# Kernel optimization log

Measured on AMD Instinct MI355X. Metric: run time of the kernel, lower is better.

The kernel has to match this reference:

```python
import jax, jax.numpy as jnp
import numpy as np
from jax import lax

B, T, P, H, L = 64, 1024, 256, 1024, 4  # batch, seq, proj(=input), cell, layers
SCALE = 1.0 / np.sqrt(H)


def _lstm_layer(x, Wih, Whh, bih, bhh, Whr):
    """One LSTM layer with projection. x: [B,T,in]. Returns h sequence [B,T,P]."""
    # Precompute input contribution to all 4 gates for all timesteps: [B,T,4H]
    xg = jnp.einsum('bti,gi->btg', x, Wih) + bih + bhh

    def step(carry, xg_t):
        h, c = carry                       # h:[B,P], c:[B,H]
        g = xg_t + h @ Whh.T               # [B,4H]
        i, f, gg, o = jnp.split(g, 4, axis=-1)  # torch gate order: i,f,g,o
        c = jax.nn.sigmoid(f) * c + jax.nn.sigmoid(i) * jnp.tanh(gg)
        h = (jax.nn.sigmoid(o) * jnp.tanh(c)) @ Whr.T  # projection -> [B,P]
        return (h, c), h

    h0 = jnp.zeros((x.shape[0], Whr.shape[0]), dtype=x.dtype)
    c0 = jnp.zeros((x.shape[0], Whr.shape[1]), dtype=x.dtype)
    _, ys = lax.scan(step, (h0, c0), jnp.swapaxes(xg, 0, 1))  # scan over time
    return jnp.swapaxes(ys, 0, 1)  # [B,T,P]


def setup_inputs() -> dict:
    key = jax.random.key(0)
    ks = jax.random.split(key, 7)
    return {
        'y': jax.random.normal(ks[0], (B, T, P), dtype=jnp.float32),
        'W_ih': jax.random.normal(ks[1], (L, 4 * H, P), dtype=jnp.float32) * SCALE,
        'W_hh': jax.random.normal(ks[2], (L, 4 * H, P), dtype=jnp.float32) * SCALE,
        'b_ih': jax.random.normal(ks[3], (L, 4 * H), dtype=jnp.float32) * SCALE,
        'b_hh': jax.random.normal(ks[4], (L, 4 * H), dtype=jnp.float32) * SCALE,
        'W_hr': jax.random.normal(ks[5], (L, P, H), dtype=jnp.float32) * SCALE,
        'min_seq_len': 1,
    }


def reference(y, W_ih, W_hh, b_ih, b_hh, W_hr, min_seq_len):
    x = y
    for l in range(L):  # small fixed layer count; dropout=0.1 is eval-mode identity
        x = _lstm_layer(x, W_ih[l], W_hh[l], b_ih[l], b_hh[l], W_hr[l])
    return x[:, min_seq_len:]
```

## Files before the change

### kernel.cpp

```cpp
#include <hip/hip_runtime.h>


#define B_    64
#define T_    1024
#define P_    256
#define H_    1024
#define L_    4
#define G4_   4096
#define NTHR  256
#define WWIN  8
#define HSLOT (P_ * B_)

#define LDS_FLOATS 37892
#define LDS_BYTES  (LDS_FLOATS * 4)

#define PA_CH  36
#define PA_BUF (64 * PA_CH)
#define PW_OFF (2 * PA_BUF)
#define PW_BUF (4 * PA_CH)

#define ACT_FLOATS ((size_t)L_ * H_ * B_)
#define WDOG_CAP 200000

struct alignas(16) F4 { float f[4]; };
typedef __attribute__((ext_vector_type(8))) short s8v;
typedef __attribute__((ext_vector_type(4))) float f4v;

__device__ __forceinline__ void lda2(const float* p, float& a, float& b) {
  union { double d; float f[2]; } u;
  u.d = __hip_atomic_load((const double*)p, __ATOMIC_RELAXED,
                          __HIP_MEMORY_SCOPE_AGENT);
  a = u.f[0]; b = u.f[1];
}
__device__ __forceinline__ void sta2(float* p, float a, float b) {
  union { double d; float f[2]; } u;
  u.f[0] = a; u.f[1] = b;
  __hip_atomic_store((double*)p, u.d, __ATOMIC_RELAXED,
                     __HIP_MEMORY_SCOPE_AGENT);
}
__device__ __forceinline__ void sta(float* p, float v) {
  __hip_atomic_store(p, v, __ATOMIC_RELAXED, __HIP_MEMORY_SCOPE_AGENT);
}
__device__ __forceinline__ void drain_vm() {
  asm volatile("s_waitcnt vmcnt(0)" ::: "memory");
}
__device__ __forceinline__ void bar_lds() {
  asm volatile("s_waitcnt lgkmcnt(0)\n\ts_barrier" ::: "memory");
}

__device__ __forceinline__ float fsig(float x) {
  float e = __expf(-x);
  return __builtin_amdgcn_rcpf(1.0f + e);
}
__device__ __forceinline__ float ftanh(float x) {
  float ax = fabsf(x);
  float e  = __expf(-2.0f * ax);
  float r  = (1.0f - e) * __builtin_amdgcn_rcpf(1.0f + e);
  return copysignf(r, x);
}
__device__ __forceinline__ ushort bf16_rne(float f) {
  uint u = __float_as_uint(f);
  uint r = u + 0x7FFFu + ((u >> 16) & 1u);
  return (ushort)(r >> 16);
}
__device__ __forceinline__ float bf16_to_f(ushort h) {
  return __uint_as_float(((uint)h) << 16);
}
__device__ __forceinline__ int wait1(int* f, int tid, int target, int* abrt,
                                     int self) {
  if (tid < 64) {
    int it = 0;
    while (true) {
      int v = (tid == self) ? 0x7fffffff
            : __hip_atomic_load(&f[tid], __ATOMIC_RELAXED, __HIP_MEMORY_SCOPE_AGENT);
      if (__ballot(v < target) == 0ull) break;
      if (++it > WDOG_CAP || *abrt) { if (tid == 0) *abrt = 1; break; }
      __builtin_amdgcn_s_sleep(2);
    }
  }
  __syncthreads();
  asm volatile("" ::: "memory");
  return *abrt;
}

extern "C" __global__ void __launch_bounds__(NTHR, 1)
lstm_persistent(const float* __restrict__ y,
                const float* __restrict__ Wih,
                const float* __restrict__ Whh,
                const float* __restrict__ bih,
                const float* __restrict__ bhh,
                const float* __restrict__ Whr,
                const int*   __restrict__ mslp,
                float*       __restrict__ out,
                float*       __restrict__ hbuf,
                float*       __restrict__ actg,
                int*         __restrict__ hflag,
                int*         __restrict__ pflag)
{
  extern __shared__ float lds[];
  ushort* WHI  = (ushort*)lds;
  ushort* WLO  = WHI + 32768;
  ushort* XS   = WLO + 32768;
  float*  ACTf = lds + 36864;
  float*  PRJ  = lds + 32768;
  int*    ABRT = (int*)(lds + 37888);

  const int bid = blockIdx.x;
  const int l   = (bid & 7) >> 1;
  const int w   = ((bid & 1)) + 2 * (bid >> 3);
  const int J0  = w * 16;
  const int tid = threadIdx.x;
  const int msl = mslp[0];

  if (tid == 0) *ABRT = 0;

  {
    const float* wih_l = Wih + (size_t)l * G4_ * P_;
    const float* whh_l = Whh + (size_t)l * G4_ * P_;
    for (int e = tid; e < 4096; e += NTHR) {
      int m  = e & 63;
      int g  = (e >> 6) & 3;
      int kt = e >> 8;
      int grow = (m & 3) * H_ + J0 + (m >> 2);
      int k = kt * 32 + g * 8;
      const float* src = (k < 256) ? (wih_l + (size_t)grow * P_ + k)
                                   : (whh_l + (size_t)grow * P_ + (k - 256));
      F4 aa = *(const F4*)src;
      F4 bb = *(const F4*)(src + 4);
      float xs8[8] = {aa.f[0], aa.f[1], aa.f[2], aa.f[3],
                      bb.f[0], bb.f[1], bb.f[2], bb.f[3]};
      s8v h8, l8;
#pragma unroll
      for (int i = 0; i < 8; ++i) {
        ushort hi = bf16_rne(xs8[i]);
        ushort lo = bf16_rne(xs8[i] - bf16_to_f(hi));
        h8[i] = (short)hi; l8[i] = (short)lo;
      }
      ((s8v*)WHI)[e] = h8;
      ((s8v*)WLO)[e] = l8;
    }
  }
  __syncthreads();

  const int w4   = tid >> 6;
  const int lane = tid & 63;
  const int gq   = lane >> 4;
  const int lm   = lane & 15;
  const int aix  = 16 * w4 + lm;
  const int cellj = 4 * w4 + gq;
  const int sb = tid >> 2;
  const int sg = tid & 3;
  const int jqr = tid >> 6, b_r = tid & 63;
  const int b_p = (w4 << 4) | (tid & 15);
  const int pw  = (tid >> 4) & 3;
  const int pws = tid >> 3, jqlw = tid & 7;

  float* hsrc = hbuf + (size_t)l * (WWIN * HSLOT);
  const float* hprv = (l > 0) ? (hbuf + (size_t)(l - 1) * (WWIN * HSLOT)) : hbuf;
  float* AGf = actg + (size_t)l * H_ * B_;

  float biasr[4];
#pragma unroll
  for (int gg = 0; gg < 4; ++gg) {
    int grow = gg * H_ + J0 + cellj;
    biasr[gg] = bih[l * G4_ + grow] + bhh[l * G4_ + grow];
  }

  float cst[4] = {0.f, 0.f, 0.f, 0.f};
  f4v acc[4];

  auto gemm_chunk = [&](int kt, int par) {
    const s8v* WHIv = (const s8v*)WHI;
    const s8v* WLOv = (const s8v*)WLO;
    s8v ahi = WHIv[(kt * 4 + gq) * 64 + aix];
    s8v alo = WLOv[(kt * 4 + gq) * 64 + aix];
    const s8v* XB = (const s8v*)XS + par * 512;
    const int bbase = gq * 64 + lm;
#pragma unroll
    for (int nt = 0; nt < 4; ++nt) {
      s8v bhi = XB[bbase + nt * 16];
      s8v blo = XB[256 + bbase + nt * 16];
      acc[nt] = __builtin_amdgcn_mfma_f32_16x16x32_bf16(ahi, bhi, acc[nt], 0, 0, 0);
      acc[nt] = __builtin_amdgcn_mfma_f32_16x16x32_bf16(ahi, blo, acc[nt], 0, 0, 0);
      acc[nt] = __builtin_amdgcn_mfma_f32_16x16x32_bf16(alo, bhi, acc[nt], 0, 0, 0);
    }
  };
  auto ring_issue = [&](const float* src, int cc, F4& u, F4& v) {
    const float* p = src + (size_t)sb * P_ + ((cc & 7) << 5) + 8 * sg;
    lda2(p + 0, u.f[0], u.f[1]);
    lda2(p + 2, u.f[2], u.f[3]);
    lda2(p + 4, v.f[0], v.f[1]);
    lda2(p + 6, v.f[2], v.f[3]);
  };
  auto commit_x = [&](int par, const F4& u, const F4& v) {
    s8v h8, l8;
#pragma unroll
    for (int i = 0; i < 4; ++i) {
      ushort hu = bf16_rne(u.f[i]);
      ushort lu = bf16_rne(u.f[i] - bf16_to_f(hu));
      ushort hv = bf16_rne(v.f[i]);
      ushort lv = bf16_rne(v.f[i] - bf16_to_f(hv));
      h8[i]     = (short)hu; l8[i]     = (short)lu;
      h8[i + 4] = (short)hv; l8[i + 4] = (short)lv;
    }
    s8v* XB = (s8v*)XS + par * 512;
    XB[sg * 64 + sb]       = h8;
    XB[256 + sg * 64 + sb] = l8;
  };
  auto run_half = [&](auto&& ISSUE, int c0) {
    F4 Au, Av, Bu, Bv;
    ISSUE(c0 + 0, Au, Av);
    ISSUE(c0 + 1, Bu, Bv);
    commit_x(0, Au, Av);
    bar_lds();
#pragma unroll
    for (int cc = 0; cc < 8; cc += 2) {
      if (cc + 2 < 8) ISSUE(c0 + cc + 2, Au, Av);
      gemm_chunk(c0 + cc, 0);
      commit_x(1, Bu, Bv);
      bar_lds();
      if (cc + 3 < 8) ISSUE(c0 + cc + 3, Bu, Bv);
      gemm_chunk(c0 + cc + 1, 1);
      if (cc + 2 < 8) commit_x(0, Au, Av);
      bar_lds();
    }
  };
  auto do_xhalf = [&](int tt) {
    f4v z = {0.f, 0.f, 0.f, 0.f};
#pragma unroll
    for (int nt = 0; nt < 4; ++nt) acc[nt] = z;
    if (l == 0) {
      auto yi = [&](int cc, F4& u, F4& v) {
        const float* p = y + ((size_t)sb * T_ + tt) * P_ + ((cc & 7) << 5) + 8 * sg;
        u = *(const F4*)p;
        v = *(const F4*)(p + 4);
      };
      run_half(yi, 0);
    } else {
      const float* xp = hprv + (size_t)(tt & (WWIN - 1)) * HSLOT;
      auto xi = [&](int cc, F4& u, F4& v) { ring_issue(xp, cc, u, v); };
      run_half(xi, 0);
    }
  };

  if (l > 0) { if (wait1(hflag + (l - 1) * 64, tid, 0, ABRT, -1)) return; }
  do_xhalf(0);

  const int cbase = w >> 1;

  for (int t = 0; t < T_; ++t) {
    if (*ABRT) return;

    if (t > 0) {
      if (wait1(hflag + l * 64, tid, t - 1, ABRT, w)) return;
      const float* hp = hsrc + (size_t)((t - 1) & (WWIN - 1)) * HSLOT;
      auto hi_ = [&](int cc, F4& u, F4& v) { ring_issue(hp, cc, u, v); };
      run_half(hi_, 8);
    }

#pragma unroll
    for (int nt = 0; nt < 4; ++nt) {
      float vi = acc[nt][0] + biasr[0];
      float vf = acc[nt][1] + biasr[1];
      float vg = acc[nt][2] + biasr[2];
      float vo = acc[nt][3] + biasr[3];
      float ig = fsig(vi), fg = fsig(vf), g2 = ftanh(vg), og = fsig(vo);
      float cn = fmaf(fg, cst[nt], ig * g2);
      cst[nt] = cn;
      ACTf[cellj * 64 + nt * 16 + lm] = og * ftanh(cn);
    }
    bar_lds();

    {
      float a0 = ACTf[(4 * jqr + 0) * 64 + b_r];
      float a1 = ACTf[(4 * jqr + 1) * 64 + b_r];
      float a2 = ACTf[(4 * jqr + 2) * 64 + b_r];
      float a3 = ACTf[(4 * jqr + 3) * 64 + b_r];
      float* dst = AGf + ((size_t)(4 * w + jqr) * 64 + b_r) * 4;
      sta2(dst + 0, a0, a1);
      sta2(dst + 2, a2, a3);
    }
    drain_vm();
    __syncthreads();
    if (tid == 0)
      __hip_atomic_store(&pflag[l * 64 + w], t, __ATOMIC_RELAXED, __HIP_MEMORY_SCOPE_AGENT);

    int* pfl = pflag + l * 64;
    auto achunk = [&](int c) { return (cbase + c) & 31; };
    auto fld = [&](int p) {
      int idx = (2 * achunk(2 * p) + (lane & 3)) & 63;
      return (idx == w) ? 0x7fffffff
           : __hip_atomic_load(&pfl[idx], __ATOMIC_RELAXED, __HIP_MEMORY_SCOPE_AGENT);
    };
    auto fver = [&](int& fv, int p) {
      int it = 0;
      while (__ballot(fv < t) != 0ull) {
        if (++it > WDOG_CAP || *ABRT) { if (tid == 0) *ABRT = 1; break; }
        __builtin_amdgcn_s_sleep(2);
        fv = fld(p);
      }
      asm volatile("" ::: "memory");
    };
    auto proj_issue = [&](int ch, F4& lo, F4& hi, F4& wv) {
      const float* a0 = AGf + ((size_t)(8 * ch + 2 * jqr) * 64 + b_r) * 4;
      lda2(a0 + 0,   lo.f[0], lo.f[1]);
      lda2(a0 + 2,   lo.f[2], lo.f[3]);
      lda2(a0 + 256, hi.f[0], hi.f[1]);
      lda2(a0 + 258, hi.f[2], hi.f[3]);
      if (tid < 32)
        wv = *(const F4*)(Whr + ((size_t)(l * P_ + 4 * w + pws)) * H_
                          + 32 * ch + 4 * jqlw);
    };
    auto proj_commit = [&](int bufi, F4& lo, F4& hi, F4& wv) {
      float* ab = PRJ + bufi * PA_BUF;
      *(F4*)&ab[b_r * PA_CH + 8 * jqr]     = lo;
      *(F4*)&ab[b_r * PA_CH + 8 * jqr + 4] = hi;
      if (tid < 32)
        *(F4*)&(PRJ + PW_OFF + bufi * PW_BUF)[pws * PA_CH + 4 * jqlw] = wv;
    };
    float s = 0.f;
    auto proj_comp = [&](int bufi) {
      const float* ab = PRJ + bufi * PA_BUF + b_p * PA_CH;
      const float* wb = PRJ + PW_OFF + bufi * PW_BUF + pw * PA_CH;
#pragma unroll
      for (int jj = 0; jj < 8; ++jj) {
        F4 a  = *(const F4*)&ab[4 * jj];
        F4 wv = *(const F4*)&wb[4 * jj];
        s = fmaf(a.f[0], wv.f[0], s);
        s = fmaf(a.f[1], wv.f[1], s);
        s = fmaf(a.f[2], wv.f[2], s);
        s = fmaf(a.f[3], wv.f[3], s);
      }
    };

    {
      int fvA = fld(0); fver(fvA, 0);
      int fvB = fld(1); fver(fvB, 1);
      F4 L0,H0,W0, L1,H1,W1, L2,H2,W2, L3,H3,W3;
      proj_issue(achunk(0), L0, H0, W0);
      proj_issue(achunk(1), L1, H1, W1);
      proj_issue(achunk(2), L2, H2, W2);
      proj_issue(achunk(3), L3, H3, W3);
      fvA = fld(2); fvB = fld(3);
      proj_commit(0, L0, H0, W0);
      bar_lds();
#pragma unroll 1
      for (int j = 0; j < 7; ++j) {
        const int c4 = 4 * j;
        fver(fvA, 2 * j + 2);
        int fvA2 = (j < 6) ? fld(2 * j + 4) : 0x7fffffff;
        proj_issue(achunk(c4 + 4), L0, H0, W0);
        proj_comp(0);
        proj_commit(1, L1, H1, W1);
        bar_lds();
        proj_issue(achunk(c4 + 5), L1, H1, W1);
        proj_comp(1);
        proj_commit(0, L2, H2, W2);
        bar_lds();
        fver(fvB, 2 * j + 3);
        int fvB2 = (j < 6) ? fld(2 * j + 5) : 0x7fffffff;
        proj_issue(achunk(c4 + 6), L2, H2, W2);
        proj_comp(0);
        proj_commit(1, L3, H3, W3);
        bar_lds();
        proj_issue(achunk(c4 + 7), L3, H3, W3);
        proj_comp(1);
        proj_commit(0, L0, H0, W0);
        bar_lds();
        fvA = fvA2; fvB = fvB2;
      }
      proj_comp(0);
      proj_commit(1, L1, H1, W1);
      bar_lds();
      proj_comp(1);
      proj_commit(0, L2, H2, W2);
      bar_lds();
      proj_comp(0);
      proj_commit(1, L3, H3, W3);
      bar_lds();
      proj_comp(1);
    }

    if (l < 3) {
      if (wait1(hflag + (l + 1) * 64, tid, t - WWIN, ABRT, -1)) return;
    }
    sta(hsrc + (size_t)(t & (WWIN - 1)) * HSLOT + (size_t)b_p * P_ + (4 * w + pw), s);
    if (l == 3 && t >= msl)
      out[((size_t)b_p * (T_ - msl) + (t - msl)) * P_ + 4 * w + pw] = s;
    drain_vm();
    __syncthreads();
    if (tid == 0)
      __hip_atomic_store(&hflag[l * 64 + w], t, __ATOMIC_RELAXED, __HIP_MEMORY_SCOPE_AGENT);

    if (t + 1 < T_) {
      if (l > 0) { if (wait1(hflag + (l - 1) * 64, tid, t + 1, ABRT, -1)) return; }
      do_xhalf(t + 1);
    }
  }
}

extern "C" void kernel_launch(void* const* d_in, const int* in_sizes, int n_in,
                              void* d_out, int out_size, void* d_ws, size_t ws_size,
                              hipStream_t stream) {
  const float* y   = (const float*)d_in[0];
  const float* Wih = (const float*)d_in[1];
  const float* Whh = (const float*)d_in[2];
  const float* bih = (const float*)d_in[3];
  const float* bhh = (const float*)d_in[4];
  const float* Whr = (const float*)d_in[5];
  const int*   msl = (const int*)d_in[6];
  float* out = (float*)d_out;

  char*  ws    = (char*)d_ws;
  int*   flags = (int*)ws;
  float* actg  = (float*)(ws + 4096);
  float* hbuf  = (float*)(ws + 4096 + ACT_FLOATS * sizeof(float));

  hipMemsetAsync(flags, 0xFF, 4096, stream);

  hipFuncSetAttribute(reinterpret_cast<const void*>(&lstm_persistent),
                      hipFuncAttributeMaxDynamicSharedMemorySize, LDS_BYTES);

  lstm_persistent<<<dim3(L_ * 64), dim3(NTHR), LDS_BYTES, stream>>>(
      y, Wih, Whh, bih, bhh, Whr, msl, out,
      hbuf, actg, flags , flags + 256 );
}
```

Measured before the change: 30.95 ms.

## Compute projection directly from registers with a single cross-wave LDS reduction

Replaces the LDS double-buffered projection stage, which staged activation chunks and Whr slices into shared memory behind a barrier per chunk, with per-thread partial dot products. Each thread keeps its loaded activations in registers, reads Whr from global or cache directly, and accumulates four projection outputs. A single LDS reduction across the four jq groups then forms the final value. This removes about 32 block barriers per timestep on the serial recurrence path, at the cost of more global weight loads per thread and extra registers.

```diff
diff --git a/kernel.cpp b/kernel.cpp
--- a/kernel.cpp
+++ b/kernel.cpp
@@ -13,11 +13,6 @@
 
 #define LDS_FLOATS 37892
 #define LDS_BYTES  (LDS_FLOATS * 4)
-
-#define PA_CH  36
-#define PA_BUF (64 * PA_CH)
-#define PW_OFF (2 * PA_BUF)
-#define PW_BUF (4 * PA_CH)
 
 #define ACT_FLOATS ((size_t)L_ * H_ * B_)
 #define WDOG_CAP 200000
@@ -102,7 +97,6 @@
   ushort* WLO  = WHI + 32768;
   ushort* XS   = WLO + 32768;
   float*  ACTf = lds + 36864;
-  float*  PRJ  = lds + 32768;
   int*    ABRT = (int*)(lds + 37888);
 
   const int bid = blockIdx.x;
@@ -153,7 +147,6 @@
   const int jqr = tid >> 6, b_r = tid & 63;
   const int b_p = (w4 << 4) | (tid & 15);
   const int pw  = (tid >> 4) & 3;
-  const int pws = tid >> 3, jqlw = tid & 7;
 
   float* hsrc = hbuf + (size_t)l * (WWIN * HSLOT);
   const float* hprv = (l > 0) ? (hbuf + (size_t)(l - 1) * (WWIN * HSLOT)) : hbuf;
@@ -247,6 +240,7 @@
   do_xhalf(0);
 
   const int cbase = w >> 1;
+  const float* whrB = Whr + ((size_t)(l * P_ + 4 * w)) * H_;
 
   for (int t = 0; t < T_; ++t) {
     if (*ABRT) return;
@@ -301,84 +295,70 @@
       }
       asm volatile("" ::: "memory");
     };
-    auto proj_issue = [&](int ch, F4& lo, F4& hi, F4& wv) {
+
+    F4 part;
+    part.f[0] = 0.f; part.f[1] = 0.f; part.f[2] = 0.f; part.f[3] = 0.f;
+    auto pissue = [&](int c, F4& lo, F4& hi) {
+      const int ch = achunk(c);
       const float* a0 = AGf + ((size_t)(8 * ch + 2 * jqr) * 64 + b_r) * 4;
       lda2(a0 + 0,   lo.f[0], lo.f[1]);
       lda2(a0 + 2,   lo.f[2], lo.f[3]);
       lda2(a0 + 256, hi.f[0], hi.f[1]);
       lda2(a0 + 258, hi.f[2], hi.f[3]);
-      if (tid < 32)
-        wv = *(const F4*)(Whr + ((size_t)(l * P_ + 4 * w + pws)) * H_
-                          + 32 * ch + 4 * jqlw);
     };
-    auto proj_commit = [&](int bufi, F4& lo, F4& hi, F4& wv) {
-      float* ab = PRJ + bufi * PA_BUF;
-      *(F4*)&ab[b_r * PA_CH + 8 * jqr]     = lo;
-      *(F4*)&ab[b_r * PA_CH + 8 * jqr + 4] = hi;
-      if (tid < 32)
-        *(F4*)&(PRJ + PW_OFF + bufi * PW_BUF)[pws * PA_CH + 4 * jqlw] = wv;
-    };
-    float s = 0.f;
-    auto proj_comp = [&](int bufi) {
-      const float* ab = PRJ + bufi * PA_BUF + b_p * PA_CH;
-      const float* wb = PRJ + PW_OFF + bufi * PW_BUF + pw * PA_CH;
-#pragma unroll
-      for (int jj = 0; jj < 8; ++jj) {
-        F4 a  = *(const F4*)&ab[4 * jj];
-        F4 wv = *(const F4*)&wb[4 * jj];
-        s = fmaf(a.f[0], wv.f[0], s);
-        s = fmaf(a.f[1], wv.f[1], s);
-        s = fmaf(a.f[2], wv.f[2], s);
-        s = fmaf(a.f[3], wv.f[3], s);
+    auto pcomp = [&](int c, F4& lo, F4& hi) {
+      const int ch = achunk(c);
+      const int j0 = 32 * ch + 8 * jqr;
+#pragma unroll
+      for (int p = 0; p < 4; ++p) {
+        F4 wa = *(const F4*)(whrB + (size_t)p * H_ + j0);
+        F4 wb = *(const F4*)(whrB + (size_t)p * H_ + j0 + 4);
+        part.f[p] = fmaf(lo.f[0], wa.f[0], part.f[p]);
+        part.f[p] = fmaf(lo.f[1], wa.f[1], part.f[p]);
+        part.f[p] = fmaf(lo.f[2], wa.f[2], part.f[p]);
+        part.f[p] = fmaf(lo.f[3], wa.f[3], part.f[p]);
+        part.f[p] = fmaf(hi.f[0], wb.f[0], part.f[p]);
+        part.f[p] = fmaf(hi.f[1], wb.f[1], part.f[p]);
+        part.f[p] = fmaf(hi.f[2], wb.f[2], part.f[p]);
+        part.f[p] = fmaf(hi.f[3], wb.f[3], part.f[p]);
       }
     };
 
     {
       int fvA = fld(0); fver(fvA, 0);
       int fvB = fld(1); fver(fvB, 1);
-      F4 L0,H0,W0, L1,H1,W1, L2,H2,W2, L3,H3,W3;
-      proj_issue(achunk(0), L0, H0, W0);
-      proj_issue(achunk(1), L1, H1, W1);
-      proj_issue(achunk(2), L2, H2, W2);
-      proj_issue(achunk(3), L3, H3, W3);
+      F4 A0l, A0h, A1l, A1h, A2l, A2h, A3l, A3h;
+      pissue(0, A0l, A0h);
+      pissue(1, A1l, A1h);
+      pissue(2, A2l, A2h);
+      pissue(3, A3l, A3h);
       fvA = fld(2); fvB = fld(3);
-      proj_commit(0, L0, H0, W0);
-      bar_lds();
 #pragma unroll 1
       for (int j = 0; j < 7; ++j) {
         const int c4 = 4 * j;
         fver(fvA, 2 * j + 2);
         int fvA2 = (j < 6) ? fld(2 * j + 4) : 0x7fffffff;
-        proj_issue(achunk(c4 + 4), L0, H0, W0);
-        proj_comp(0);
-        proj_commit(1, L1, H1, W1);
-        bar_lds();
-        proj_issue(achunk(c4 + 5), L1, H1, W1);
-        proj_comp(1);
-        proj_commit(0, L2, H2, W2);
-        bar_lds();
+        pcomp(c4 + 0, A0l, A0h); pissue(c4 + 4, A0l, A0h);
+        pcomp(c4 + 1, A1l, A1h); pissue(c4 + 5, A1l, A1h);
         fver(fvB, 2 * j + 3);
         int fvB2 = (j < 6) ? fld(2 * j + 5) : 0x7fffffff;
-        proj_issue(achunk(c4 + 6), L2, H2, W2);
-        proj_comp(0);
-        proj_commit(1, L3, H3, W3);
-        bar_lds();
-        proj_issue(achunk(c4 + 7), L3, H3, W3);
-        proj_comp(1);
-        proj_commit(0, L0, H0, W0);
-        bar_lds();
+        pcomp(c4 + 2, A2l, A2h); pissue(c4 + 6, A2l, A2h);
+        pcomp(c4 + 3, A3l, A3h); pissue(c4 + 7, A3l, A3h);
         fvA = fvA2; fvB = fvB2;
       }
-      proj_comp(0);
-      proj_commit(1, L1, H1, W1);
+      pcomp(28, A0l, A0h);
+      pcomp(29, A1l, A1h);
+      pcomp(30, A2l, A2h);
+      pcomp(31, A3l, A3h);
+    }
+
+    float s;
+    {
+      float* RED = ACTf;
+      *(F4*)&RED[tid * 4] = part;
       bar_lds();
-      proj_comp(1);
-      proj_commit(0, L2, H2, W2);
-      bar_lds();
-      proj_comp(0);
-      proj_commit(1, L3, H3, W3);
-      bar_lds();
-      proj_comp(1);
+      s = RED[(0 * 64 + b_p) * 4 + pw] + RED[(1 * 64 + b_p) * 4 + pw]
+        + RED[(2 * 64 + b_p) * 4 + pw] + RED[(3 * 64 + b_p) * 4 + pw];
     }
 
     if (l < 3) {
```

Result: faster. 30.19 ms (-2.5%).
